# Kernel optimization log

Hardware: AMD Instinct MI355X
Metric: run time of the kernel (lower is better)

Reference implementation:

```python
import jax, jax.numpy as jnp
import numpy as np

B, T, N, U = 64, 128, 128, 128  # batch, seq_len, n_features, lstm units


def setup_inputs() -> dict:
    key = jax.random.key(0)
    ks = jax.random.split(key, 8)
    s = 0.05
    return {
        "x": jax.random.normal(ks[0], (B, T, N), dtype=jnp.float32),
        "hidden_state": jnp.zeros((B, U), jnp.float32),
        "cell_state": jnp.zeros((B, U), jnp.float32),
        "lstm_kernel": jax.random.normal(ks[1], (N, 4 * U), jnp.float32) * s,
        "lstm_bias": jnp.zeros((4 * U,), jnp.float32),
        "w1_kernel": jax.random.normal(ks[2], (1, T), jnp.float32) * s,
        "w1_bias": jnp.zeros((T,), jnp.float32),
        "w2_kernel": jax.random.normal(ks[3], (2 * U, T), jnp.float32) * s,
        "w2_bias": jnp.zeros((T,), jnp.float32),
        "v_kernel": jax.random.normal(ks[4], (T, 1), jnp.float32) * s,
        "v_bias": jnp.zeros((1,), jnp.float32),
        "n": N,
    }


def reference(x, hidden_state, cell_state, lstm_kernel, lstm_bias,
              w1_kernel, w1_bias, w2_kernel, w2_bias, v_kernel, v_bias, n):
    # NewLSTM ignores the provided initial state, so every timestep's LSTM
    # runs a length-1 sequence from zero (h, c). No recurrence -> vectorize
    # over time. Keras gate order: i, f, c(g), o; recurrent kernel * 0 drops out.
    z = x @ lstm_kernel + lstm_bias                       # (B,T,4U)
    i, f, g, o = jnp.split(z, 4, axis=-1)
    c = jax.nn.sigmoid(i) * jnp.tanh(g)                   # f-gate * c_prev(=0) vanishes
    h = jax.nn.sigmoid(o) * jnp.tanh(c)                   # (B,T,U)

    # Input attention per timestep, vectorized over T.
    query = jnp.concatenate([h, c], axis=-1)              # (B,T,2U)
    s2 = query @ w2_kernel + w2_bias                      # (B,T,T)
    # w1 is Dense(T) on a size-1 feature axis: x_scalar * w1_kernel[0] + b.
    s1 = x[..., None] * w1_kernel[0] + w1_bias            # (B,T,N,T)
    score = jnp.tanh(s1 + s2[:, :, None, :])              # (B,T,N,T)
    e = jnp.einsum('btnk,k->btn', score, v_kernel[:, 0]) + v_bias[0]  # (B,T,N)
    alpha = jax.nn.softmax(e, axis=-1)                    # softmax over features

    return x * alpha                                      # (B,T,N)
```

## Files before the change

kernel.cpp:

```cpp
#include <hip/hip_runtime.h>
#include <math.h>


typedef __attribute__((ext_vector_type(8))) short short8;
typedef __attribute__((ext_vector_type(4))) float f32x4;

#define BT 8192
#define NF 128
#define XP 132
#define FP 17
#define K_C     2.8853900817779268f
#define K_LOG2E 1.4426950408889634f

__device__ __forceinline__ float fast_rcp(float x)  { return __builtin_amdgcn_rcpf(x); }
__device__ __forceinline__ float fast_exp2(float x) { return __builtin_amdgcn_exp2f(x); }

__device__ __forceinline__ float tanh_nc(float tC) {
    return fmaf(-2.f, fast_rcp(1.f + fast_exp2(tC)), 1.f);
}
__device__ __forceinline__ float tanh_fast(float t) { return tanh_nc(t * K_C); }
__device__ __forceinline__ float sig_fast(float z) {
    return fast_rcp(1.f + fast_exp2(-K_LOG2E * z));
}
__device__ __forceinline__ unsigned short f2bf(float f) {
    unsigned u = __float_as_uint(f);
    return (unsigned short)((u + 0x7fffu + ((u >> 16) & 1u)) >> 16);
}

__global__ __launch_bounds__(64) void prep(const float* __restrict__ Wl,
                                           const float* __restrict__ w2,
                                           unsigned short* __restrict__ wsB) {
    const int lane = threadIdx.x;
    const int n16 = lane & 15, q = lane >> 4;
    const int b = blockIdx.x;
    if (b < 96) {
        const int nt = b >> 2, kk = b & 3;
        const int g = nt >> 3, jt = nt & 7;
        const int goff = (g == 0) ? 0 : (g == 1 ? 256 : 384);
        const int col = goff + jt * 16 + n16;
        unsigned short* d = wsB + b * 512 + lane * 8;
        #pragma unroll
        for (int j = 0; j < 8; j++)
            d[j] = f2bf(Wl[(kk * 32 + q * 8 + j) * 512 + col]);
    } else {
        const int fs = b - 96;
        const int nt2 = fs >> 3, kk2 = fs & 7;
        const int col = nt2 * 16 + n16;
        unsigned short* d = wsB + 49152 + fs * 512 + lane * 8;
        #pragma unroll
        for (int j = 0; j < 8; j++)
            d[j] = f2bf(w2[(kk2 * 32 + q * 8 + j) * 128 + col]);
    }
}

__global__ __launch_bounds__(256, 4) void enc(
    const float* __restrict__ x,  const unsigned short* __restrict__ wsB,
    const float* __restrict__ bl, const float* __restrict__ b2,
    const float* __restrict__ b1, const float* __restrict__ w1,
    const float* __restrict__ v,  float* __restrict__ out)
{
    __shared__ __align__(16) float xs[16][XP];
    __shared__ unsigned short Qf[8 * 512];
    __shared__ __align__(16) float c2[16][XP];
    __shared__ __align__(16) float w1Cs[NF], vs[NF];
    __shared__ float Ftab[16][FP];
    __shared__ float rowMn[16], rowMx[16];

    const int t    = threadIdx.x;
    const int lane = t & 63, w = t >> 6;
    const int n16  = lane & 15, q = lane >> 4;
    const int rowbase = blockIdx.x * 16;

    {
        const int row = t >> 4, c8 = (t & 15) * 8;
        const float4 a = *(const float4*)(x + (rowbase + row) * NF + c8);
        const float4 b = *(const float4*)(x + (rowbase + row) * NF + c8 + 4);
        *(float4*)&xs[row][c8]     = a;
        *(float4*)&xs[row][c8 + 4] = b;
        float mn = fminf(fminf(a.x, a.y), fminf(a.z, a.w));
        float mx = fmaxf(fmaxf(a.x, a.y), fmaxf(a.z, a.w));
        mn = fminf(mn, fminf(fminf(b.x, b.y), fminf(b.z, b.w)));
        mx = fmaxf(mx, fmaxf(fmaxf(b.x, b.y), fmaxf(b.z, b.w)));
        #pragma unroll
        for (int off = 1; off < 16; off <<= 1) {
            mn = fminf(mn, __shfl_xor(mn, off, 16));
            mx = fmaxf(mx, __shfl_xor(mx, off, 16));
        }
        if ((t & 15) == 0) { rowMn[row] = mn; rowMx[row] = mx; }
    }
    if (t < NF) { w1Cs[t] = w1[t] * K_C; vs[t] = v[t]; }
    __syncthreads();

    short8 af[4];
    #pragma unroll
    for (int kk = 0; kk < 4; kk++) {
        const float4 v0 = *(const float4*)&xs[n16][kk * 32 + q * 8];
        const float4 v1 = *(const float4*)&xs[n16][kk * 32 + q * 8 + 4];
        short8 a;
        a[0] = f2bf(v0.x); a[1] = f2bf(v0.y); a[2] = f2bf(v0.z); a[3] = f2bf(v0.w);
        a[4] = f2bf(v1.x); a[5] = f2bf(v1.y); a[6] = f2bf(v1.z); a[7] = f2bf(v1.w);
        af[kk] = a;
    }

    f32x4 acc[2][3];
    #pragma unroll
    for (int j2 = 0; j2 < 2; j2++)
        #pragma unroll
        for (int g = 0; g < 3; g++) acc[j2][g] = (f32x4)(0.f);
    const short8* B1g = (const short8*)wsB;
    short8 bcur[2][3], bnxt[2][3];
    #pragma unroll
    for (int j2 = 0; j2 < 2; j2++)
        #pragma unroll
        for (int g = 0; g < 3; g++)
            bcur[j2][g] = B1g[((g * 8 + (w * 2 + j2)) * 4 + 0) * 64 + lane];
    #pragma unroll
    for (int kk = 0; kk < 4; kk++) {
        if (kk < 3)
            #pragma unroll
            for (int j2 = 0; j2 < 2; j2++)
                #pragma unroll
                for (int g = 0; g < 3; g++)
                    bnxt[j2][g] = B1g[((g * 8 + (w * 2 + j2)) * 4 + kk + 1) * 64 + lane];
        #pragma unroll
        for (int j2 = 0; j2 < 2; j2++)
            #pragma unroll
            for (int g = 0; g < 3; g++)
                acc[j2][g] = __builtin_amdgcn_mfma_f32_16x16x32_bf16(
                    af[kk], bcur[j2][g], acc[j2][g], 0, 0, 0);
        #pragma unroll
        for (int j2 = 0; j2 < 2; j2++)
            #pragma unroll
            for (int g = 0; g < 3; g++) bcur[j2][g] = bnxt[j2][g];
    }

    #pragma unroll
    for (int j2 = 0; j2 < 2; j2++) {
        const int u = (w * 2 + j2) * 16 + n16;
        const float bi = bl[u], bg = bl[256 + u], bo = bl[384 + u];
        const int kqh = u, kqc = NF + u;
        const int baseh = (kqh >> 5) * 512 + ((kqh & 31) >> 3) * 128 + q * 32 + (kqh & 7);
        const int basec = (kqc >> 5) * 512 + ((kqc & 31) >> 3) * 128 + q * 32 + (kqc & 7);
        #pragma unroll
        for (int r = 0; r < 4; r++) {
            const float c = sig_fast(acc[j2][0][r] + bi) * tanh_fast(acc[j2][1][r] + bg);
            const float h = sig_fast(acc[j2][2][r] + bo) * tanh_fast(c);
            Qf[baseh + r * 8] = f2bf(h);
            Qf[basec + r * 8] = f2bf(c);
        }
    }
    __syncthreads();

    {
        short8 a2[8];
        #pragma unroll
        for (int kk2 = 0; kk2 < 8; kk2++)
            a2[kk2] = *(const short8*)&Qf[kk2 * 512 + lane * 8];
        const short8* B2g = (const short8*)(wsB + 49152);
        #pragma unroll
        for (int j2 = 0; j2 < 2; j2++) {
            const int nt2 = w * 2 + j2;
            short8 bf[8];
            #pragma unroll
            for (int kk2 = 0; kk2 < 8; kk2++)
                bf[kk2] = B2g[(nt2 * 8 + kk2) * 64 + lane];
            f32x4 acc2 = (f32x4)(0.f);
            #pragma unroll
            for (int kk2 = 0; kk2 < 8; kk2++)
                acc2 = __builtin_amdgcn_mfma_f32_16x16x32_bf16(a2[kk2], bf[kk2], acc2, 0, 0, 0);
            const int u2 = nt2 * 16 + n16;
            const float bias2 = (b2[u2] + b1[u2]) * K_C;
            #pragma unroll
            for (int r = 0; r < 4; r++)
                c2[q * 4 + r][u2] = fmaf(acc2[r], K_C, bias2);
        }
    }
    __syncthreads();

    {
        const int row = t >> 4;
        const int m   = t & 15;
        const float mn = rowMn[row];
        const float h  = (rowMx[row] - mn) * (1.f / 13.f);
        const float xi = fmaf((float)(m - 1), h, mn);
        float accF = 0.f;
        #pragma unroll 4
        for (int k = 0; k < NF; k += 4) {
            const float4 w4 = *(const float4*)&w1Cs[k];
            const float4 c4 = *(const float4*)&c2[row][k];
            const float4 v4 = *(const float4*)&vs[k];
            accF = fmaf(tanh_nc(fmaf(xi, w4.x, c4.x)), v4.x, accF);
            accF = fmaf(tanh_nc(fmaf(xi, w4.y, c4.y)), v4.y, accF);
            accF = fmaf(tanh_nc(fmaf(xi, w4.z, c4.z)), v4.z, accF);
            accF = fmaf(tanh_nc(fmaf(xi, w4.w, c4.w)), v4.w, accF);
        }
        Ftab[row][m] = accF;
    }
    __syncthreads();

    {
        const int row = t >> 4;
        const int n0  = (t & 15) * 8;
        const float mn   = rowMn[row];
        const float span = rowMx[row] - mn;
        const float invh = span > 1e-12f ? 13.f / span : 0.f;
        float xv[8], e8[8];
        *(float4*)&xv[0] = *(const float4*)&xs[row][n0];
        *(float4*)&xv[4] = *(const float4*)&xs[row][n0 + 4];
        #pragma unroll
        for (int i = 0; i < 8; i++) {
            const float sN = fmaf(xv[i] - mn, invh, 1.0f);
            int ii = (int)sN;
            ii = ii < 1 ? 1 : (ii > 13 ? 13 : ii);
            const float f  = sN - (float)ii;
            const float F0 = Ftab[row][ii - 1], F1 = Ftab[row][ii];
            const float F2 = Ftab[row][ii + 1], F3 = Ftab[row][ii + 2];
            e8[i] = F1 + 0.5f * f * ((F2 - F0)
                  + f * ((2.f * F0 - 5.f * F1 + 4.f * F2 - F3)
                  + f * (3.f * (F1 - F2) + F3 - F0)));
        }
        float mval = e8[0];
        #pragma unroll
        for (int i = 1; i < 8; i++) mval = fmaxf(mval, e8[i]);
        #pragma unroll
        for (int off = 1; off < 16; off <<= 1)
            mval = fmaxf(mval, __shfl_xor(mval, off, 16));
        float ssum = 0.f;
        #pragma unroll
        for (int i = 0; i < 8; i++) {
            e8[i] = fast_exp2(K_LOG2E * (e8[i] - mval));
            ssum += e8[i];
        }
        #pragma unroll
        for (int off = 1; off < 16; off <<= 1)
            ssum += __shfl_xor(ssum, off, 16);
        const float rs = fast_rcp(ssum);
        float4 o0, o1;
        o0.x = xv[0] * e8[0] * rs; o0.y = xv[1] * e8[1] * rs;
        o0.z = xv[2] * e8[2] * rs; o0.w = xv[3] * e8[3] * rs;
        o1.x = xv[4] * e8[4] * rs; o1.y = xv[5] * e8[5] * rs;
        o1.z = xv[6] * e8[6] * rs; o1.w = xv[7] * e8[7] * rs;
        float* op = out + (rowbase + row) * NF + n0;
        *(float4*)op       = o0;
        *(float4*)(op + 4) = o1;
    }
}

extern "C" void kernel_launch(void* const* d_in, const int* in_sizes, int n_in,
                              void* d_out, int out_size, void* d_ws, size_t ws_size,
                              hipStream_t stream) {
    const float* x  = (const float*)d_in[0];
    const float* Wl = (const float*)d_in[3];
    const float* bl = (const float*)d_in[4];
    const float* w1 = (const float*)d_in[5];
    const float* b1 = (const float*)d_in[6];
    const float* w2 = (const float*)d_in[7];
    const float* b2 = (const float*)d_in[8];
    const float* v  = (const float*)d_in[9];
    float* out = (float*)d_out;
    unsigned short* wsB = (unsigned short*)d_ws;

    prep<<<160, 64, 0, stream>>>(Wl, w2, wsB);
    enc<<<BT / 16, 256, 0, stream>>>(x, wsB, bl, b2, b1, w1, v, out);
}
```

Baseline: 88.04 us.

## Process 32 rows per block with 8 waves, each reusing its weight fragments

Result: no change. 87.33 us (-0.8%).

```diff
diff --git a/kernel.cpp b/kernel.cpp
--- a/kernel.cpp
+++ b/kernel.cpp
@@ -53,126 +53,115 @@
     }
 }
 
-__global__ __launch_bounds__(256, 4) void enc(
+__global__ __launch_bounds__(512, 2) void enc(
     const float* __restrict__ x,  const unsigned short* __restrict__ wsB,
     const float* __restrict__ bl, const float* __restrict__ b2,
     const float* __restrict__ b1, const float* __restrict__ w1,
     const float* __restrict__ v,  float* __restrict__ out)
 {
-    __shared__ __align__(16) float xs[16][XP];
-    __shared__ unsigned short Qf[8 * 512];
-    __shared__ __align__(16) float c2[16][XP];
+    __shared__ __align__(16) float xs[32][XP];
+    __shared__ unsigned short Qf[2][4096];
+    __shared__ __align__(16) float c2[32][XP];
     __shared__ __align__(16) float w1Cs[NF], vs[NF];
-    __shared__ float Ftab[16][FP];
-    __shared__ float rowMn[16], rowMx[16];
+    __shared__ float Ftab[32][FP];
+    __shared__ float rowMn[32], rowMx[32];
 
     const int t    = threadIdx.x;
     const int lane = t & 63, w = t >> 6;
     const int n16  = lane & 15, q = lane >> 4;
-    const int rowbase = blockIdx.x * 16;
-
-    {
-        const int row = t >> 4, c8 = (t & 15) * 8;
-        const float4 a = *(const float4*)(x + (rowbase + row) * NF + c8);
-        const float4 b = *(const float4*)(x + (rowbase + row) * NF + c8 + 4);
-        *(float4*)&xs[row][c8]     = a;
-        *(float4*)&xs[row][c8 + 4] = b;
+    const int rowbase = blockIdx.x * 32;
+
+    const short8* B1g = (const short8*)wsB;
+    short8 b1f[3][4];
+    #pragma unroll
+    for (int g = 0; g < 3; g++)
+        #pragma unroll
+        for (int kk = 0; kk < 4; kk++)
+            b1f[g][kk] = B1g[((g * 8 + w) * 4 + kk) * 64 + lane];
+
+    #pragma unroll
+    for (int p = 0; p < 2; p++) {
+        const int i   = t + p * 512;
+        const int row = i >> 5, col = (i & 31) * 4;
+        const float4 a = *(const float4*)(x + (rowbase + row) * NF + col);
+        *(float4*)&xs[row][col] = a;
         float mn = fminf(fminf(a.x, a.y), fminf(a.z, a.w));
         float mx = fmaxf(fmaxf(a.x, a.y), fmaxf(a.z, a.w));
-        mn = fminf(mn, fminf(fminf(b.x, b.y), fminf(b.z, b.w)));
-        mx = fmaxf(mx, fmaxf(fmaxf(b.x, b.y), fmaxf(b.z, b.w)));
-        #pragma unroll
-        for (int off = 1; off < 16; off <<= 1) {
-            mn = fminf(mn, __shfl_xor(mn, off, 16));
-            mx = fmaxf(mx, __shfl_xor(mx, off, 16));
-        }
-        if ((t & 15) == 0) { rowMn[row] = mn; rowMx[row] = mx; }
+        #pragma unroll
+        for (int off = 1; off < 32; off <<= 1) {
+            mn = fminf(mn, __shfl_xor(mn, off, 32));
+            mx = fmaxf(mx, __shfl_xor(mx, off, 32));
+        }
+        if ((t & 31) == 0) { rowMn[row] = mn; rowMx[row] = mx; }
     }
     if (t < NF) { w1Cs[t] = w1[t] * K_C; vs[t] = v[t]; }
     __syncthreads();
 
-    short8 af[4];
-    #pragma unroll
-    for (int kk = 0; kk < 4; kk++) {
-        const float4 v0 = *(const float4*)&xs[n16][kk * 32 + q * 8];
-        const float4 v1 = *(const float4*)&xs[n16][kk * 32 + q * 8 + 4];
-        short8 a;
-        a[0] = f2bf(v0.x); a[1] = f2bf(v0.y); a[2] = f2bf(v0.z); a[3] = f2bf(v0.w);
-        a[4] = f2bf(v1.x); a[5] = f2bf(v1.y); a[6] = f2bf(v1.z); a[7] = f2bf(v1.w);
-        af[kk] = a;
-    }
+    short8 af[2][4];
+    #pragma unroll
+    for (int c = 0; c < 2; c++)
+        #pragma unroll
+        for (int kk = 0; kk < 4; kk++) {
+            const float4 v0 = *(const float4*)&xs[c * 16 + n16][kk * 32 + q * 8];
+            const float4 v1 = *(const float4*)&xs[c * 16 + n16][kk * 32 + q * 8 + 4];
+            short8 a;
+            a[0] = f2bf(v0.x); a[1] = f2bf(v0.y); a[2] = f2bf(v0.z); a[3] = f2bf(v0.w);
+            a[4] = f2bf(v1.x); a[5] = f2bf(v1.y); a[6] = f2bf(v1.z); a[7] = f2bf(v1.w);
+            af[c][kk] = a;
+        }
 
     f32x4 acc[2][3];
     #pragma unroll
-    for (int j2 = 0; j2 < 2; j2++)
-        #pragma unroll
-        for (int g = 0; g < 3; g++) acc[j2][g] = (f32x4)(0.f);
-    const short8* B1g = (const short8*)wsB;
-    short8 bcur[2][3], bnxt[2][3];
-    #pragma unroll
-    for (int j2 = 0; j2 < 2; j2++)
-        #pragma unroll
-        for (int g = 0; g < 3; g++)
-            bcur[j2][g] = B1g[((g * 8 + (w * 2 + j2)) * 4 + 0) * 64 + lane];
-    #pragma unroll
-    for (int kk = 0; kk < 4; kk++) {
-        if (kk < 3)
-            #pragma unroll
-            for (int j2 = 0; j2 < 2; j2++)
-                #pragma unroll
-                for (int g = 0; g < 3; g++)
-                    bnxt[j2][g] = B1g[((g * 8 + (w * 2 + j2)) * 4 + kk + 1) * 64 + lane];
-        #pragma unroll
-        for (int j2 = 0; j2 < 2; j2++)
+    for (int c = 0; c < 2; c++)
+        #pragma unroll
+        for (int g = 0; g < 3; g++) acc[c][g] = (f32x4)(0.f);
+    #pragma unroll
+    for (int kk = 0; kk < 4; kk++)
+        #pragma unroll
+        for (int c = 0; c < 2; c++)
             #pragma unroll
             for (int g = 0; g < 3; g++)
-                acc[j2][g] = __builtin_amdgcn_mfma_f32_16x16x32_bf16(
-                    af[kk], bcur[j2][g], acc[j2][g], 0, 0, 0);
-        #pragma unroll
-        for (int j2 = 0; j2 < 2; j2++)
-            #pragma unroll
-            for (int g = 0; g < 3; g++) bcur[j2][g] = bnxt[j2][g];
-    }
-
-    #pragma unroll
-    for (int j2 = 0; j2 < 2; j2++) {
-        const int u = (w * 2 + j2) * 16 + n16;
+                acc[c][g] = __builtin_amdgcn_mfma_f32_16x16x32_bf16(
+                    af[c][kk], b1f[g][kk], acc[c][g], 0, 0, 0);
+
+    const int u = w * 16 + n16;
+    {
         const float bi = bl[u], bg = bl[256 + u], bo = bl[384 + u];
         const int kqh = u, kqc = NF + u;
         const int baseh = (kqh >> 5) * 512 + ((kqh & 31) >> 3) * 128 + q * 32 + (kqh & 7);
         const int basec = (kqc >> 5) * 512 + ((kqc & 31) >> 3) * 128 + q * 32 + (kqc & 7);
         #pragma unroll
-        for (int r = 0; r < 4; r++) {
-            const float c = sig_fast(acc[j2][0][r] + bi) * tanh_fast(acc[j2][1][r] + bg);
-            const float h = sig_fast(acc[j2][2][r] + bo) * tanh_fast(c);
-            Qf[baseh + r * 8] = f2bf(h);
-            Qf[basec + r * 8] = f2bf(c);
-        }
-    }
-    __syncthreads();
-
-    {
-        short8 a2[8];
+        for (int c = 0; c < 2; c++)
+            #pragma unroll
+            for (int r = 0; r < 4; r++) {
+                const float cc = sig_fast(acc[c][0][r] + bi) * tanh_fast(acc[c][1][r] + bg);
+                const float hh = sig_fast(acc[c][2][r] + bo) * tanh_fast(cc);
+                Qf[c][baseh + r * 8] = f2bf(hh);
+                Qf[c][basec + r * 8] = f2bf(cc);
+            }
+    }
+    __syncthreads();
+
+    {
+        const short8* B2g = (const short8*)(wsB + 49152);
+        short8 b2f[8];
         #pragma unroll
         for (int kk2 = 0; kk2 < 8; kk2++)
-            a2[kk2] = *(const short8*)&Qf[kk2 * 512 + lane * 8];
-        const short8* B2g = (const short8*)(wsB + 49152);
-        #pragma unroll
-        for (int j2 = 0; j2 < 2; j2++) {
-            const int nt2 = w * 2 + j2;
-            short8 bf[8];
+            b2f[kk2] = B2g[(w * 8 + kk2) * 64 + lane];
+        const float bias2 = (b2[u] + b1[u]) * K_C;
+        #pragma unroll
+        for (int c = 0; c < 2; c++) {
+            short8 a2[8];
             #pragma unroll
             for (int kk2 = 0; kk2 < 8; kk2++)
-                bf[kk2] = B2g[(nt2 * 8 + kk2) * 64 + lane];
+                a2[kk2] = *(const short8*)&Qf[c][kk2 * 512 + lane * 8];
             f32x4 acc2 = (f32x4)(0.f);
             #pragma unroll
             for (int kk2 = 0; kk2 < 8; kk2++)
-                acc2 = __builtin_amdgcn_mfma_f32_16x16x32_bf16(a2[kk2], bf[kk2], acc2, 0, 0, 0);
-            const int u2 = nt2 * 16 + n16;
-            const float bias2 = (b2[u2] + b1[u2]) * K_C;
+                acc2 = __builtin_amdgcn_mfma_f32_16x16x32_bf16(a2[kk2], b2f[kk2], acc2, 0, 0, 0);
             #pragma unroll
             for (int r = 0; r < 4; r++)
-                c2[q * 4 + r][u2] = fmaf(acc2[r], K_C, bias2);
+                c2[c * 16 + q * 4 + r][u] = fmaf(acc2[r], K_C, bias2);
         }
     }
     __syncthreads();
@@ -261,5 +250,5 @@
     unsigned short* wsB = (unsigned short*)d_ws;
 
     prep<<<160, 64, 0, stream>>>(Wl, w2, wsB);
-    enc<<<BT / 16, 256, 0, stream>>>(x, wsB, bl, b2, b1, w1, v, out);
-}
+    enc<<<BT / 32, 512, 0, stream>>>(x, wsB, bl, b2, b1, w1, v, out);
+}
```
